# Kernel tuning notes

Measured on AMD Instinct MI355X. Metric: run time of the kernel, lower is better.

## Reference

```python
import jax, jax.numpy as jnp
import numpy as np

N_NODES = 50000
N_EDGES = 500000
IN_DIM = 256
HEADS = 4
OUT_C = 64
NEG_SLOPE = 0.2


def setup_inputs() -> dict:
    key = jax.random.key(0)
    ks = jax.random.split(key, 6)
    x = jax.random.normal(ks[0], (N_NODES, IN_DIM), dtype=jnp.float32)
    edge_index = jax.random.randint(ks[1], (2, N_EDGES), 0, N_NODES, dtype=jnp.int64)
    scale = 1.0 / np.sqrt(IN_DIM)
    W_l = jax.random.normal(ks[2], (IN_DIM, HEADS * OUT_C), dtype=jnp.float32) * scale
    W_r = jax.random.normal(ks[3], (IN_DIM, HEADS * OUT_C), dtype=jnp.float32) * scale
    b_l = jnp.zeros((HEADS * OUT_C,), dtype=jnp.float32)
    b_r = jnp.zeros((HEADS * OUT_C,), dtype=jnp.float32)
    att = jax.random.normal(ks[4], (HEADS, OUT_C), dtype=jnp.float32) * (1.0 / np.sqrt(OUT_C))
    bias = jnp.zeros((HEADS * OUT_C,), dtype=jnp.float32)
    return {"x": x, "edge_index": edge_index, "W_l": W_l, "b_l": b_l,
            "W_r": W_r, "b_r": b_r, "att": att, "bias": bias}


def _gatv2(x, edge_index, W_l, b_l, W_r, b_r, att, bias):
    N = x.shape[0]
    H, C = att.shape
    # add self loops (PyG GATv2Conv default add_self_loops=True)
    loop = jnp.arange(N, dtype=edge_index.dtype)
    src = jnp.concatenate([edge_index[0], loop])  # message sources (x_j)
    dst = jnp.concatenate([edge_index[1], loop])  # aggregation targets (x_i)
    x_l = (x @ W_l + b_l).reshape(N, H, C)  # source-side projection
    x_r = (x @ W_r + b_r).reshape(N, H, C)  # target-side projection
    # GATv2 attention logits: a^T LeakyReLU(x_l[src] + x_r[dst])
    e = jax.nn.leaky_relu(x_l[src] + x_r[dst], NEG_SLOPE)  # [E, H, C]
    logits = jnp.einsum('ehc,hc->eh', e, att)              # [E, H]
    # segmented softmax over incoming edges of each dst node
    m = jax.ops.segment_max(logits, dst, num_segments=N)   # [N, H]
    ex = jnp.exp(logits - m[dst])
    denom = jax.ops.segment_sum(ex, dst, num_segments=N)   # [N, H]
    alpha = ex / denom[dst]                                # [E, H]
    # weighted scatter-aggregation of source messages
    out = jax.ops.segment_sum(x_l[src] * alpha[:, :, None], dst, num_segments=N)  # [N, H, C]
    return out.reshape(N, H * C) + bias


def reference(x, edge_index, W_l, b_l, W_r, b_r, att, bias):
    out = _gatv2(x, edge_index, W_l, b_l, W_r, b_r, att, bias)  # [N, H*C]
    # wrapper: single relation -> reshape(-1, 1, output_dim) and cat on dim=1
    return out.reshape(-1, 1, HEADS * OUT_C)
```

## Files before the change

### kernel.cpp

```cpp
#include <hip/hip_runtime.h>
#include <hip/hip_bf16.h>
#include <math.h>

#define N_NODES 50000
#define N_PAD   50048
#define N_EDGES 500000
#define E_TOT   550000
#define HC      256
#define NHC     512
#define HEADS   4
#define NEG     0.2f

typedef __attribute__((ext_vector_type(8))) short short8;
typedef __attribute__((ext_vector_type(4))) float f32x4;
typedef __attribute__((ext_vector_type(2))) float f32x2;

__device__ __forceinline__ ushort f2bf(float f) {
    union { float f; unsigned u; } c; c.f = f;
    unsigned u = c.u;
    unsigned rounded = u + 0x7FFFu + ((u >> 16) & 1u);
    return (ushort)(rounded >> 16);
}

static constexpr size_t OFF_COUNTS = 0;
static constexpr size_t OFF_CUR    = OFF_COUNTS + (size_t)N_NODES * 4;
static constexpr size_t OFF_ROWS   = OFF_CUR + (size_t)N_NODES * 4;
static constexpr size_t OFF_SRCS   = OFF_ROWS + (size_t)(N_NODES + 1) * 4;
static constexpr size_t OFF_BSUM   = OFF_SRCS + (size_t)E_TOT * 4;
static constexpr size_t OFF_MODE   = OFF_BSUM + 64 * 4;
static constexpr size_t OFF_XB     = ((OFF_MODE + 4 + 255) / 256) * 256;
static constexpr size_t OFF_WT     = OFF_XB + (size_t)N_PAD * HC * 2;
static constexpr size_t OFF_XLB    = OFF_WT + (size_t)NHC * HC * 2;
static constexpr size_t OFF_XRB    = OFF_XLB + (size_t)N_NODES * HC * 2;

__device__ __forceinline__ int get_src(const int* __restrict__ ei, int mode, int e) {
    if (e >= N_EDGES) return e - N_EDGES;
    return mode ? ei[2 * e] : ei[e];
}
__device__ __forceinline__ int get_dst(const int* __restrict__ ei, int mode, int e) {
    if (e >= N_EDGES) return e - N_EDGES;
    return mode ? ei[2 * (N_EDGES + e)] : ei[N_EDGES + e];
}

#define XBLK 6256
#define WBLK 512
__global__ __launch_bounds__(256) void prep_kernel(
        const float* __restrict__ x, const float* __restrict__ Wl,
        const float* __restrict__ Wr, const int* __restrict__ ei,
        ushort* __restrict__ xb, ushort* __restrict__ wt, int* __restrict__ mode) {
    const int b = blockIdx.x;
    if (b < XBLK) {
        size_t i = ((size_t)b * 256 + threadIdx.x) * 8;
        if (i >= (size_t)N_PAD * HC) return;
        ushort o[8];
        if (i < (size_t)N_NODES * HC) {
            float4 v0 = *(const float4*)(x + i);
            float4 v1 = *(const float4*)(x + i + 4);
            o[0] = f2bf(v0.x); o[1] = f2bf(v0.y); o[2] = f2bf(v0.z); o[3] = f2bf(v0.w);
            o[4] = f2bf(v1.x); o[5] = f2bf(v1.y); o[6] = f2bf(v1.z); o[7] = f2bf(v1.w);
        } else {
#pragma unroll
            for (int j = 0; j < 8; ++j) o[j] = 0;
        }
        *(short8*)(xb + i) = *(short8*)o;
    } else if (b < XBLK + WBLK) {
        int i = (b - XBLK) * 256 + threadIdx.x;
        int n = i >> 8, k = i & 255;
        float v = (n < HC) ? Wl[(size_t)k * HC + n] : Wr[(size_t)k * HC + (n - HC)];
        wt[i] = f2bf(v);
    } else {
        __shared__ int any;
        if (threadIdx.x == 0) any = 0;
        __syncthreads();
        if (ei[2 * threadIdx.x + 1] != 0) atomicOr(&any, 1);
        __syncthreads();
        if (threadIdx.x == 0) mode[0] = (any == 0) ? 1 : 0;
    }
}

#define BM 128
#define BK 32
__global__ __launch_bounds__(256) void mfma_gemm_kernel(
        const __hip_bfloat16* __restrict__ xb, const __hip_bfloat16* __restrict__ wt,
        const float* __restrict__ bl, const float* __restrict__ br,
        ushort* __restrict__ xlb, ushort* __restrict__ xrb) {
    __shared__ __hip_bfloat16 As[2][BM * BK];
    __shared__ __hip_bfloat16 Bs[2][BM * BK];
    const int t    = threadIdx.x;
    const int lane = t & 63;
    const int wid  = t >> 6;
    const int wr   = wid >> 1, wc = wid & 1;
    const int brow = blockIdx.x * BM;
    const int bcol = blockIdx.y * BM;

    auto stage = [&](int buf, int k0) {
#pragma unroll
        for (int r = 0; r < 2; ++r) {
            int c = r * 256 + t;
            const __hip_bfloat16* ga = xb + ((size_t)(brow + (c >> 2)) * HC + k0 + (c & 3) * 8);
            __builtin_amdgcn_global_load_lds(
                (const __attribute__((address_space(1))) void*)ga,
                (__attribute__((address_space(3))) void*)((char*)&As[buf][0] + c * 16),
                16, 0, 0);
        }
#pragma unroll
        for (int r = 0; r < 2; ++r) {
            int c = r * 256 + t;
            const __hip_bfloat16* gb = wt + ((size_t)(bcol + (c >> 2)) * HC + k0 + (c & 3) * 8);
            __builtin_amdgcn_global_load_lds(
                (const __attribute__((address_space(1))) void*)gb,
                (__attribute__((address_space(3))) void*)((char*)&Bs[buf][0] + c * 16),
                16, 0, 0);
        }
    };

    f32x4 acc[4][4];
#pragma unroll
    for (int m = 0; m < 4; ++m)
#pragma unroll
        for (int n = 0; n < 4; ++n) acc[m][n] = (f32x4)0.f;

    stage(0, 0);
    __syncthreads();

    const int rsub = lane & 15;
    const int koff = (lane >> 4) * 16;

    for (int kk = 0; kk < 8; ++kk) {
        const int cur = kk & 1;
        if (kk < 7) stage(cur ^ 1, (kk + 1) * BK);
        short8 a[4], b[4];
#pragma unroll
        for (int m = 0; m < 4; ++m)
            a[m] = *(const short8*)((const char*)&As[cur][0] +
                    (wr * 64 + m * 16 + rsub) * (BK * 2) + koff);
#pragma unroll
        for (int n = 0; n < 4; ++n)
            b[n] = *(const short8*)((const char*)&Bs[cur][0] +
                    (wc * 64 + n * 16 + rsub) * (BK * 2) + koff);
#pragma unroll
        for (int m = 0; m < 4; ++m)
#pragma unroll
            for (int n = 0; n < 4; ++n)
                acc[m][n] = __builtin_amdgcn_mfma_f32_16x16x32_bf16(a[m], b[n], acc[m][n], 0, 0, 0);
        __syncthreads();
    }

    ushort* dst = (bcol < HC) ? xlb : xrb;
    const float* bvec = (bcol < HC) ? bl : br;
    const int cb = bcol & (HC - 1);
#pragma unroll
    for (int m = 0; m < 4; ++m) {
#pragma unroll
        for (int n = 0; n < 4; ++n) {
            int col = cb + wc * 64 + n * 16 + (lane & 15);
            float bv = bvec[col];
#pragma unroll
            for (int j = 0; j < 4; ++j) {
                int row = brow + wr * 64 + m * 16 + (lane >> 4) * 4 + j;
                if (row < N_NODES) dst[(size_t)row * HC + col] = f2bf(acc[m][n][j] + bv);
            }
        }
    }
}

__global__ void count_kernel(const int* __restrict__ ei, const int* __restrict__ mode,
                             int* __restrict__ counts) {
    int e = blockIdx.x * blockDim.x + threadIdx.x;
    if (e < E_TOT) atomicAdd(&counts[get_dst(ei, *mode, e)], 1);
}

__global__ void scan1_kernel(const int* __restrict__ counts, int* __restrict__ rows,
                             int* __restrict__ bsum) {
    __shared__ int sdata[256];
    const int t = threadIdx.x;
    const int base = blockIdx.x * 1024 + t * 4;
    int v[4]; int s = 0;
#pragma unroll
    for (int j = 0; j < 4; ++j) {
        int idx = base + j;
        v[j] = (idx < N_NODES) ? counts[idx] : 0;
        s += v[j];
    }
    sdata[t] = s;
    __syncthreads();
    for (int off = 1; off < 256; off <<= 1) {
        int xv = (t >= off) ? sdata[t - off] : 0;
        __syncthreads();
        sdata[t] += xv;
        __syncthreads();
    }
    int run = sdata[t] - s;
#pragma unroll
    for (int j = 0; j < 4; ++j) {
        int idx = base + j;
        if (idx < N_NODES) rows[idx] = run;
        run += v[j];
    }
    if (t == 255) bsum[blockIdx.x] = sdata[255];
}

__global__ void scan2_kernel(int* __restrict__ bsum, int* __restrict__ rows) {
    if (threadIdx.x == 0 && blockIdx.x == 0) {
        int run = 0;
        for (int b = 0; b < 49; ++b) { int xv = bsum[b]; bsum[b] = run; run += xv; }
        rows[N_NODES] = E_TOT;
    }
}

__global__ void scan3_kernel(int* __restrict__ rows, const int* __restrict__ bsum) {
    int idx = blockIdx.x * 256 + threadIdx.x;
    if (idx < N_NODES) rows[idx] += bsum[idx >> 10];
}

__global__ void fill_kernel(const int* __restrict__ ei, const int* __restrict__ mode,
                            const int* __restrict__ rows, int* __restrict__ cursor,
                            int* __restrict__ srcs) {
    int e = blockIdx.x * blockDim.x + threadIdx.x;
    if (e < E_TOT) {
        int md = *mode;
        int d = get_dst(ei, md, e);
        int s = get_src(ei, md, e);
        int pos = atomicAdd(&cursor[d], 1);
        srcs[rows[d] + pos] = s;
    }
}

__global__ __launch_bounds__(256) void fused_agg_kernel(
        const ushort* __restrict__ xlb, const ushort* __restrict__ xrb,
        const float* __restrict__ att,
        const int* __restrict__ rows, const int* __restrict__ srcs,
        const float* __restrict__ bias, float* __restrict__ out) {
    const int lane = threadIdx.x & 63;
    const int n = (blockIdx.x * 256 + threadIdx.x) >> 6;
    if (n >= N_NODES) return;
    const int half = lane >> 5;
    const int sl   = lane & 31;
    const int start = rows[n], end = rows[n + 1];

    f32x2 xr2[4], at2[4];
    {
        uint4 c = *(const uint4*)(xrb + (size_t)n * HC + sl * 8);
        unsigned w[4] = {c.x, c.y, c.z, c.w};
#pragma unroll
        for (int j = 0; j < 4; ++j) {
            xr2[j][0] = __uint_as_float(w[j] << 16);
            xr2[j][1] = __uint_as_float(w[j] & 0xffff0000u);
        }
        float4 a0 = *(const float4*)&att[sl * 8];
        float4 a1 = *(const float4*)&att[sl * 8 + 4];
        at2[0][0] = a0.x; at2[0][1] = a0.y; at2[1][0] = a0.z; at2[1][1] = a0.w;
        at2[2][0] = a1.x; at2[2][1] = a1.y; at2[3][0] = a1.z; at2[3][1] = a1.w;
    }

    f32x2 acc2[4];
#pragma unroll
    for (int j = 0; j < 4; ++j) acc2[j] = (f32x2)0.f;
    float sm = 0.f;

    int i = start + half;
    uint4 rA = make_uint4(0, 0, 0, 0);
    int sB = -1;
    if (i < end) rA = *(const uint4*)(xlb + (size_t)srcs[i] * HC + sl * 8);
    if (i + 2 < end) sB = srcs[i + 2];

    for (; i < end; i += 2) {
        uint4 r = rA;
        if (sB >= 0) rA = *(const uint4*)(xlb + (size_t)sB * HC + sl * 8);
        sB = (i + 4 < end) ? srcs[i + 4] : -1;

        unsigned w[4] = {r.x, r.y, r.z, r.w};
        f32x2 xv[4];
#pragma unroll
        for (int j = 0; j < 4; ++j) {
            xv[j][0] = __uint_as_float(w[j] << 16);
            xv[j][1] = __uint_as_float(w[j] & 0xffff0000u);
        }

        f32x2 p2 = (f32x2)0.f;
#pragma unroll
        for (int j = 0; j < 4; ++j) {
            f32x2 v = xv[j] + xr2[j];
            f32x2 lk = __builtin_elementwise_max(v, v * NEG);
            p2 = lk * at2[j] + p2;
        }
        float p = p2[0] + p2[1];
        p += __shfl_xor(p, 1, 64);
        p += __shfl_xor(p, 2, 64);
        p += __shfl_xor(p, 4, 64);

        float wgt = __expf(p);
        sm += wgt;
        f32x2 w2; w2[0] = wgt; w2[1] = wgt;
#pragma unroll
        for (int j = 0; j < 4; ++j) acc2[j] = xv[j] * w2 + acc2[j];
    }

    sm += __shfl_xor(sm, 32, 64);
#pragma unroll
    for (int j = 0; j < 4; ++j) {
        acc2[j][0] += __shfl_xor(acc2[j][0], 32, 64);
        acc2[j][1] += __shfl_xor(acc2[j][1], 32, 64);
    }

    if (half == 0) {
        const float inv = 1.0f / sm;
        float4 b0 = *(const float4*)&bias[sl * 8];
        float4 b1 = *(const float4*)&bias[sl * 8 + 4];
        float4 o0, o1;
        o0.x = fmaf(acc2[0][0], inv, b0.x); o0.y = fmaf(acc2[0][1], inv, b0.y);
        o0.z = fmaf(acc2[1][0], inv, b0.z); o0.w = fmaf(acc2[1][1], inv, b0.w);
        o1.x = fmaf(acc2[2][0], inv, b1.x); o1.y = fmaf(acc2[2][1], inv, b1.y);
        o1.z = fmaf(acc2[3][0], inv, b1.z); o1.w = fmaf(acc2[3][1], inv, b1.w);
        *(float4*)&out[(size_t)n * HC + sl * 8]     = o0;
        *(float4*)&out[(size_t)n * HC + sl * 8 + 4] = o1;
    }
}

extern "C" void kernel_launch(void* const* d_in, const int* in_sizes, int n_in,
                              void* d_out, int out_size, void* d_ws, size_t ws_size,
                              hipStream_t stream) {
    const float* x    = (const float*)d_in[0];
    const int*   ei   = (const int*)d_in[1];
    const float* Wl   = (const float*)d_in[2];
    const float* bl   = (const float*)d_in[3];
    const float* Wr   = (const float*)d_in[4];
    const float* br   = (const float*)d_in[5];
    const float* att  = (const float*)d_in[6];
    const float* bias = (const float*)d_in[7];
    float* out = (float*)d_out;

    char* ws = (char*)d_ws;
    int*   counts = (int*)(ws + OFF_COUNTS);
    int*   cursor = (int*)(ws + OFF_CUR);
    int*   rows   = (int*)(ws + OFF_ROWS);
    int*   srcs   = (int*)(ws + OFF_SRCS);
    int*   bsum   = (int*)(ws + OFF_BSUM);
    int*   mode   = (int*)(ws + OFF_MODE);
    ushort* xb    = (ushort*)(ws + OFF_XB);
    ushort* wt    = (ushort*)(ws + OFF_WT);
    ushort* xlb   = (ushort*)(ws + OFF_XLB);
    ushort* xrb   = (ushort*)(ws + OFF_XRB);

    (void)hipMemsetAsync(counts, 0, (size_t)N_NODES * 8, stream);

    prep_kernel<<<XBLK + WBLK + 1, 256, 0, stream>>>(x, Wl, Wr, ei, xb, wt, mode);

    dim3 ggrid(N_PAD / BM, NHC / BM);
    mfma_gemm_kernel<<<ggrid, 256, 0, stream>>>(
        (const __hip_bfloat16*)xb, (const __hip_bfloat16*)wt, bl, br, xlb, xrb);

    count_kernel<<<(E_TOT + 255) / 256, 256, 0, stream>>>(ei, mode, counts);
    scan1_kernel<<<49, 256, 0, stream>>>(counts, rows, bsum);
    scan2_kernel<<<1, 64, 0, stream>>>(bsum, rows);
    scan3_kernel<<<(N_NODES + 255) / 256, 256, 0, stream>>>(rows, bsum);
    fill_kernel<<<(E_TOT + 255) / 256, 256, 0, stream>>>(ei, mode, rows, cursor, srcs);

    fused_agg_kernel<<<(N_NODES + 3) / 4, 256, 0, stream>>>(
        xlb, xrb, att, rows, srcs, bias, out);
}
```

Before: 169.6 us.

## Stage GEMM epilogue through swizzled LDS, deepen gather prefetch, fold memset into prep

```diff
diff --git a/kernel.cpp b/kernel.cpp
--- a/kernel.cpp
+++ b/kernel.cpp
@@ -44,10 +44,12 @@
 
 #define XBLK 6256
 #define WBLK 512
+#define ZBLK 98
 __global__ __launch_bounds__(256) void prep_kernel(
         const float* __restrict__ x, const float* __restrict__ Wl,
         const float* __restrict__ Wr, const int* __restrict__ ei,
-        ushort* __restrict__ xb, ushort* __restrict__ wt, int* __restrict__ mode) {
+        ushort* __restrict__ xb, ushort* __restrict__ wt,
+        int* __restrict__ cz, int* __restrict__ mode) {
     const int b = blockIdx.x;
     if (b < XBLK) {
         size_t i = ((size_t)b * 256 + threadIdx.x) * 8;
@@ -68,6 +70,9 @@
         int n = i >> 8, k = i & 255;
         float v = (n < HC) ? Wl[(size_t)k * HC + n] : Wr[(size_t)k * HC + (n - HC)];
         wt[i] = f2bf(v);
+    } else if (b < XBLK + WBLK + ZBLK) {
+        int i4 = (b - XBLK - WBLK) * 256 + threadIdx.x;
+        if (i4 < 2 * N_NODES / 4) *(int4*)(cz + i4 * 4) = make_int4(0, 0, 0, 0);
     } else {
         __shared__ int any;
         if (threadIdx.x == 0) any = 0;
@@ -84,8 +89,9 @@
         const __hip_bfloat16* __restrict__ xb, const __hip_bfloat16* __restrict__ wt,
         const float* __restrict__ bl, const float* __restrict__ br,
         ushort* __restrict__ xlb, ushort* __restrict__ xrb) {
-    __shared__ __hip_bfloat16 As[2][BM * BK];
-    __shared__ __hip_bfloat16 Bs[2][BM * BK];
+    __shared__ ushort smem[4 * BM * BK];
+    auto AS = [&](int buf) { return (__hip_bfloat16*)(smem + buf * BM * BK); };
+    auto BS = [&](int buf) { return (__hip_bfloat16*)(smem + 2 * BM * BK + buf * BM * BK); };
     const int t    = threadIdx.x;
     const int lane = t & 63;
     const int wid  = t >> 6;
@@ -100,7 +106,7 @@
             const __hip_bfloat16* ga = xb + ((size_t)(brow + (c >> 2)) * HC + k0 + (c & 3) * 8);
             __builtin_amdgcn_global_load_lds(
                 (const __attribute__((address_space(1))) void*)ga,
-                (__attribute__((address_space(3))) void*)((char*)&As[buf][0] + c * 16),
+                (__attribute__((address_space(3))) void*)((char*)AS(buf) + c * 16),
                 16, 0, 0);
         }
 #pragma unroll
@@ -109,7 +115,7 @@
             const __hip_bfloat16* gb = wt + ((size_t)(bcol + (c >> 2)) * HC + k0 + (c & 3) * 8);
             __builtin_amdgcn_global_load_lds(
                 (const __attribute__((address_space(1))) void*)gb,
-                (__attribute__((address_space(3))) void*)((char*)&Bs[buf][0] + c * 16),
+                (__attribute__((address_space(3))) void*)((char*)BS(buf) + c * 16),
                 16, 0, 0);
         }
     };
@@ -132,11 +138,11 @@
         short8 a[4], b[4];
 #pragma unroll
         for (int m = 0; m < 4; ++m)
-            a[m] = *(const short8*)((const char*)&As[cur][0] +
+            a[m] = *(const short8*)((const char*)AS(cur) +
                     (wr * 64 + m * 16 + rsub) * (BK * 2) + koff);
 #pragma unroll
         for (int n = 0; n < 4; ++n)
-            b[n] = *(const short8*)((const char*)&Bs[cur][0] +
+            b[n] = *(const short8*)((const char*)BS(cur) +
                     (wc * 64 + n * 16 + rsub) * (BK * 2) + koff);
 #pragma unroll
         for (int m = 0; m < 4; ++m)
@@ -153,12 +159,26 @@
     for (int m = 0; m < 4; ++m) {
 #pragma unroll
         for (int n = 0; n < 4; ++n) {
-            int col = cb + wc * 64 + n * 16 + (lane & 15);
-            float bv = bvec[col];
+            int c_loc = wc * 64 + n * 16 + (lane & 15);
+            float bv = bvec[cb + c_loc];
 #pragma unroll
             for (int j = 0; j < 4; ++j) {
-                int row = brow + wr * 64 + m * 16 + (lane >> 4) * 4 + j;
-                if (row < N_NODES) dst[(size_t)row * HC + col] = f2bf(acc[m][n][j] + bv);
+                int r_loc = wr * 64 + m * 16 + (lane >> 4) * 4 + j;
+                smem[r_loc * 128 + (((c_loc >> 3) ^ (r_loc & 15)) * 8) + (c_loc & 7)] =
+                    f2bf(acc[m][n][j] + bv);
+            }
+        }
+    }
+    __syncthreads();
+    {
+        const int r = t >> 1, hf = t & 1;
+        if (brow + r < N_NODES) {
+            ushort* gout = dst + (size_t)(brow + r) * HC + cb + hf * 64;
+#pragma unroll
+            for (int i = 0; i < 8; ++i) {
+                int ci = hf * 8 + i;
+                uint4 v = *(const uint4*)&smem[r * 128 + ((ci ^ (r & 15)) * 8)];
+                *(uint4*)(gout + i * 8) = v;
             }
         }
     }
@@ -259,15 +279,17 @@
     float sm = 0.f;
 
     int i = start + half;
-    uint4 rA = make_uint4(0, 0, 0, 0);
-    int sB = -1;
-    if (i < end) rA = *(const uint4*)(xlb + (size_t)srcs[i] * HC + sl * 8);
-    if (i + 2 < end) sB = srcs[i + 2];
+    uint4 rA = make_uint4(0, 0, 0, 0), rB = make_uint4(0, 0, 0, 0);
+    int sC = -1;
+    if (i < end)     rA = *(const uint4*)(xlb + (size_t)srcs[i] * HC + sl * 8);
+    if (i + 2 < end) rB = *(const uint4*)(xlb + (size_t)srcs[i + 2] * HC + sl * 8);
+    if (i + 4 < end) sC = srcs[i + 4];
 
     for (; i < end; i += 2) {
         uint4 r = rA;
-        if (sB >= 0) rA = *(const uint4*)(xlb + (size_t)sB * HC + sl * 8);
-        sB = (i + 4 < end) ? srcs[i + 4] : -1;
+        rA = rB;
+        if (sC >= 0) rB = *(const uint4*)(xlb + (size_t)sC * HC + sl * 8);
+        sC = (i + 6 < end) ? srcs[i + 6] : -1;
 
         unsigned w[4] = {r.x, r.y, r.z, r.w};
         f32x2 xv[4];
@@ -342,9 +364,8 @@
     ushort* xlb   = (ushort*)(ws + OFF_XLB);
     ushort* xrb   = (ushort*)(ws + OFF_XRB);
 
-    (void)hipMemsetAsync(counts, 0, (size_t)N_NODES * 8, stream);
-
-    prep_kernel<<<XBLK + WBLK + 1, 256, 0, stream>>>(x, Wl, Wr, ei, xb, wt, mode);
+    prep_kernel<<<XBLK + WBLK + ZBLK + 1, 256, 0, stream>>>(
+        x, Wl, Wr, ei, xb, wt, counts, mode);
 
     dim3 ggrid(N_PAD / BM, NHC / BM);
     mfma_gemm_kernel<<<ggrid, 256, 0, stream>>>(
```

After: 166.2 us. 2.0% less time.
